# Performance work log

Hardware: AMD Instinct MI355X
Metric: run time of the kernel (lower is better)

## Reference

```python
import jax, jax.numpy as jnp
import numpy as np

EMBED = 1024
HEADS = 16
HEAD_DIM = EMBED // HEADS


def setup_inputs() -> dict:
    key = jax.random.key(0)
    ks = jax.random.split(key, 12)
    N, S, E = 4, 2048, EMBED
    scale = 1.0 / np.sqrt(E)
    inp = {
        "values": jax.random.normal(ks[0], (N, S, E), dtype=jnp.float32),
        "keys": jax.random.normal(ks[1], (N, S, E), dtype=jnp.float32),
        "query": jax.random.normal(ks[2], (N, S, E), dtype=jnp.float32),
        "mask": jnp.ones((N, 1, 1, S), dtype=jnp.int32),
        # Linear params: y = x @ W + b (W stored as [in, out])
        "Wv": jax.random.normal(ks[3], (E, E), dtype=jnp.float32) * scale,
        "bv": jnp.zeros((E,), dtype=jnp.float32),
        "Wk": jax.random.normal(ks[4], (E, E), dtype=jnp.float32) * scale,
        "bk": jnp.zeros((E,), dtype=jnp.float32),
        "Wq": jax.random.normal(ks[5], (E, E), dtype=jnp.float32) * scale,
        "bq": jnp.zeros((E,), dtype=jnp.float32),
        "Wo": jax.random.normal(ks[6], (E, E), dtype=jnp.float32) * scale,
        "bo": jnp.zeros((E,), dtype=jnp.float32),
    }
    return inp


def reference(values, keys, query, mask, Wv, bv, Wk, bk, Wq, bq, Wo, bo):
    N, Q, E = query.shape
    V = values.shape[1]
    K = keys.shape[1]
    v = (values @ Wv + bv).reshape(N, V, HEADS, HEAD_DIM)
    k = (keys @ Wk + bk).reshape(N, K, HEADS, HEAD_DIM)
    q = (query @ Wq + bq).reshape(N, Q, HEADS, HEAD_DIM)
    # energy: [N, H, Q, K]
    energy = jnp.einsum("nqhd,nkhd->nhqk", q, k)
    energy = jnp.where(mask == 0, jnp.float32(-1e20), energy)
    # NOTE: original scales by sqrt(embed_size), not sqrt(head_dim)
    attn = jax.nn.softmax(energy / jnp.sqrt(jnp.float32(E)), axis=3)
    out = jnp.einsum("nhql,nlhd->nqhd", attn, v).reshape(N, Q, E)
    return out @ Wo + bo
```

## Files before the change

### kernel.cpp

```cpp
#include <hip/hip_runtime.h>

#define H 16
#define DH 64
#define S 2048
#define E 1024
#define NB 4

typedef short short8_t __attribute__((ext_vector_type(8)));
typedef float float4_t __attribute__((ext_vector_type(4)));
typedef float float16_t __attribute__((ext_vector_type(16)));

__device__ inline unsigned short f2bf(float f) {
    union { float f; unsigned u; } v; v.f = f;
    unsigned r = v.u + 0x7fffu + ((v.u >> 16) & 1u);
    return (unsigned short)(r >> 16);
}

__device__ __forceinline__ unsigned pk_bf16(float a, float b) {
    union { float f; unsigned u; } ua, ub;
    ua.f = a; ub.f = b;
    unsigned ra = ua.u + 0x7fffu + ((ua.u >> 16) & 1u);
    unsigned rb = ub.u + 0x7fffu + ((ub.u >> 16) & 1u);
    return __builtin_amdgcn_perm(rb, ra, 0x07060302u);
}

__device__ __forceinline__ unsigned cvt_pk_bf16(float a, float b) {
    unsigned r;
    asm("v_cvt_pk_bf16_f32 %0, %1, %2" : "=v"(r) : "v"(a), "v"(b));
    return r;
}

__device__ __forceinline__ float16_t mfma32(short8_t a, short8_t b, float16_t c) {
    return __builtin_amdgcn_mfma_f32_32x32x16_bf16(a, b, c, 0, 0, 0);
}

__device__ __forceinline__ void async_copy16(const unsigned short* g, unsigned short* l) {
    __builtin_amdgcn_global_load_lds(
        (const __attribute__((address_space(1))) unsigned int*)g,
        (__attribute__((address_space(3))) unsigned int*)l, 16, 0, 0);
}

__global__ __launch_bounds__(256) void xcvt_kernel(
    const float* __restrict__ v, const float* __restrict__ k,
    const float* __restrict__ q, unsigned short* __restrict__ xv,
    unsigned short* __restrict__ xk, unsigned short* __restrict__ xq)
{
    const int z = blockIdx.y;
    const float* src = (z == 0) ? v : (z == 1) ? k : q;
    unsigned short* dst = (z == 0) ? xv : (z == 1) ? xk : xq;
    size_t i0 = ((size_t)blockIdx.x * 256 + threadIdx.x) * 8;
    float4 f0 = *reinterpret_cast<const float4*>(src + i0);
    float4 f1 = *reinterpret_cast<const float4*>(src + i0 + 4);
    uint4 o;
    o.x = pk_bf16(f0.x, f0.y); o.y = pk_bf16(f0.z, f0.w);
    o.z = pk_bf16(f1.x, f1.y); o.w = pk_bf16(f1.z, f1.w);
    *reinterpret_cast<uint4*>(dst + i0) = o;
}

__global__ __launch_bounds__(256) void wcvt_kernel(
    const float* __restrict__ Wv, const float* __restrict__ Wk,
    const float* __restrict__ Wq, const float* __restrict__ Wo,
    unsigned short* __restrict__ Wt)
{
    __shared__ float tile[64][65];
    const float* W = (blockIdx.z == 0) ? Wv : (blockIdx.z == 1) ? Wk
                   : (blockIdx.z == 2) ? Wq : Wo;
    unsigned short* out = Wt + (size_t)blockIdx.z * (E * E);
    const int k0 = blockIdx.x * 64, n0 = blockIdx.y * 64;
    const int tid = threadIdx.x;
#pragma unroll
    for (int i = 0; i < 4; ++i) {
        int c = i * 256 + tid;
        int kl = c >> 4, nl4 = (c & 15) * 4;
        float4 v = *reinterpret_cast<const float4*>(W + (size_t)(k0 + kl) * E + n0 + nl4);
        tile[kl][nl4 + 0] = v.x; tile[kl][nl4 + 1] = v.y;
        tile[kl][nl4 + 2] = v.z; tile[kl][nl4 + 3] = v.w;
    }
    __syncthreads();
#pragma unroll
    for (int i = 0; i < 4; ++i) {
        int c = i * 256 + tid;
        int nl = c >> 4, kl4 = (c & 15) * 4;
        ushort4 o;
        o.x = f2bf(tile[kl4 + 0][nl]); o.y = f2bf(tile[kl4 + 1][nl]);
        o.z = f2bf(tile[kl4 + 2][nl]); o.w = f2bf(tile[kl4 + 3][nl]);
        *reinterpret_cast<ushort4*>(out + (size_t)(n0 + nl) * E + k0 + kl4) = o;
    }
}

template<int MODE>
__global__ __launch_bounds__(256) void proj_kernel(
    const unsigned short* __restrict__ A, const unsigned short* __restrict__ WT,
    const float* __restrict__ bias, unsigned short* __restrict__ out)
{
    __shared__ __align__(16) unsigned short As[2][128][64];
    __shared__ __align__(16) unsigned short Bs[2][128][64];

    const int tid = threadIdx.x;
    const int m0 = blockIdx.y * 128;
    const int n0 = blockIdx.x * 128;
    const int wave = tid >> 6, lane = tid & 63;
    const int wm = wave >> 1, wn = wave & 1;
    const int quad = lane >> 4, l16 = lane & 15;
    const int r8 = lane >> 3;
    const int c8 = (lane & 7) ^ (r8 & 7);

    float4_t acc[4][4];
#pragma unroll
    for (int i = 0; i < 4; ++i)
#pragma unroll
        for (int j = 0; j < 4; ++j) { float4_t z = {0.f,0.f,0.f,0.f}; acc[i][j] = z; }

#pragma unroll
    for (int j = 0; j < 4; ++j) {
        int row = wave * 32 + j * 8 + r8;
        async_copy16(A  + (size_t)(m0 + row) * E + c8 * 8, &As[0][wave * 32 + j * 8][0]);
        async_copy16(WT + (size_t)(n0 + row) * E + c8 * 8, &Bs[0][wave * 32 + j * 8][0]);
    }

    for (int it = 0; it < 16; ++it) {
        const int cur = it & 1, nxt = cur ^ 1;
        __syncthreads();

        if (it < 15) {
            const int kn = (it + 1) * 64;
#pragma unroll
            for (int j = 0; j < 4; ++j) {
                int row = wave * 32 + j * 8 + r8;
                async_copy16(A  + (size_t)(m0 + row) * E + kn + c8 * 8, &As[nxt][wave * 32 + j * 8][0]);
                async_copy16(WT + (size_t)(n0 + row) * E + kn + c8 * 8, &Bs[nxt][wave * 32 + j * 8][0]);
            }
        }
#pragma unroll
        for (int kk = 0; kk < 2; ++kk) {
            short8_t a[4], b[4];
#pragma unroll
            for (int mi = 0; mi < 4; ++mi)
                a[mi] = *reinterpret_cast<const short8_t*>(
                    &As[cur][wm * 64 + mi * 16 + l16][((kk * 4 + quad) ^ (l16 & 7)) * 8]);
#pragma unroll
            for (int nj = 0; nj < 4; ++nj)
                b[nj] = *reinterpret_cast<const short8_t*>(
                    &Bs[cur][wn * 64 + nj * 16 + l16][((kk * 4 + quad) ^ (l16 & 7)) * 8]);
#pragma unroll
            for (int x = 0; x < 4; ++x)
#pragma unroll
                for (int y = 0; y < 4; ++y) {
                    if (MODE == 0)
                        acc[x][y] = __builtin_amdgcn_mfma_f32_16x16x32_bf16(b[x], a[y], acc[x][y], 0, 0, 0);
                    else
                        acc[x][y] = __builtin_amdgcn_mfma_f32_16x16x32_bf16(a[x], b[y], acc[x][y], 0, 0, 0);
                }
        }
    }

    if (MODE == 0) {
#pragma unroll
        for (int x = 0; x < 4; ++x) {
            float4 bb = *reinterpret_cast<const float4*>(&bias[n0 + wn * 64 + x * 16 + quad * 4]);
#pragma unroll
            for (int y = 0; y < 4; ++y) {
                int m = m0 + wm * 64 + y * 16 + l16;
                int nn = m >> 11, s = m & 2047;
#pragma unroll
                for (int r = 0; r < 4; ++r) {
                    int gcol = n0 + wn * 64 + x * 16 + quad * 4 + r;
                    int h = gcol >> 6, d = gcol & 63;
                    float val = acc[x][y][r] + ((const float*)&bb)[r];
                    out[(((size_t)(nn * H + h)) * DH + d) * S + s] = f2bf(val);
                }
            }
        }
    } else {
#pragma unroll
        for (int x = 0; x < 4; ++x) {
#pragma unroll
            for (int y = 0; y < 4; ++y) {
                int gcol = n0 + wn * 64 + y * 16 + l16;
                float bvv = bias[gcol];
                int h = gcol >> 6, d = gcol & 63;
#pragma unroll
                for (int r = 0; r < 4; ++r) {
                    int gm = m0 + wm * 64 + x * 16 + quad * 4 + r;
                    float val = acc[x][y][r] + bvv;
                    int nn = gm >> 11, s = gm & 2047;
                    out[(((size_t)(nn * H + h)) * S + s) * DH + d] = f2bf(val);
                }
            }
        }
    }
}

__global__ __launch_bounds__(256, 4) void flash_kernel(
    const unsigned short* __restrict__ Qb, const unsigned short* __restrict__ Kb,
    const unsigned short* __restrict__ VTb, const int* __restrict__ mask,
    unsigned short* __restrict__ AO)
{
    __shared__ __align__(16) unsigned short Ks[2][64][64];
    __shared__ __align__(16) unsigned short Vs[2][64][64];
    __shared__ __align__(16) float am[2][64];
    __shared__ __align__(16) float lbuf[4][32];

    const int tid = threadIdx.x;
    const int wave = tid >> 6, lane = tid & 63;
    const int l32 = lane & 31, hf = lane >> 5;
    const int r8 = lane >> 3;
    const int c8 = (lane & 7) ^ (r8 & 7);

    const int wlin = blockIdx.y * 16 + blockIdx.x;
    const int wid = (wlin & 7) * 128 + (wlin >> 3);
    const int qt = wid & 15;
    const int nh = wid >> 4;
    const int n = nh >> 4, h = nh & 15;
    const size_t hb = (size_t)nh * S * DH;
    const unsigned short* Qh = Qb + hb;
    const unsigned short* Kh = Kb + hb;
    const unsigned short* Vh = VTb + hb;
    const int* mp = mask + n * S;

    const float c1 = 0.03125f * 1.4426950408889634f;
    const float C2_UNMASK = -23.083120654223414f;
    const float C2_MASK   = -1.44e20f;

    short8_t qa[4];
#pragma unroll
    for (int ks = 0; ks < 4; ++ks) {
        int row = qt * 128 + wave * 32 + l32;
        qa[ks] = *reinterpret_cast<const short8_t*>(Qh + (size_t)row * DH + ks * 16 + hf * 8);
    }

    float16_t o[2];
#pragma unroll
    for (int nb = 0; nb < 2; ++nb)
#pragma unroll
        for (int i = 0; i < 16; ++i) o[nb][i] = 0.f;
    float lsum = 0.f;

#pragma unroll
    for (int j = 0; j < 2; ++j) {
        int row = wave * 16 + j * 8 + r8;
        async_copy16(Kh + (size_t)row * DH + c8 * 8, &Ks[0][wave * 16 + j * 8][0]);
        async_copy16(Vh + (size_t)row * S + c8 * 8,  &Vs[0][wave * 16 + j * 8][0]);
    }
    if (tid < 64) am[0][tid] = (mp[tid] == 0) ? C2_MASK : C2_UNMASK;

    for (int it = 0; it < 32; ++it) {
        const int cur = it & 1, nxt = cur ^ 1;
        __syncthreads();

        const int kn = (it < 31) ? (it + 1) * 64 : 0;
#pragma unroll
        for (int j = 0; j < 2; ++j) {
            int row = wave * 16 + j * 8 + r8;
            async_copy16(Kh + (size_t)(kn + row) * DH + c8 * 8, &Ks[nxt][wave * 16 + j * 8][0]);
            async_copy16(Vh + (size_t)row * S + kn + c8 * 8,    &Vs[nxt][wave * 16 + j * 8][0]);
        }
        if (tid < 64) am[nxt][tid] = (mp[kn + tid] == 0) ? C2_MASK : C2_UNMASK;

        unsigned w[2][4][2];
#pragma unroll
        for (int kvb = 0; kvb < 2; ++kvb) {
            float16_t st;
#pragma unroll
            for (int i = 0; i < 16; ++i) st[i] = 0.f;
            __builtin_amdgcn_s_setprio(1);
#pragma unroll
            for (int ks = 0; ks < 4; ++ks) {
                short8_t ak = *reinterpret_cast<const short8_t*>(
                    &Ks[cur][kvb * 32 + l32][((ks * 2 + hf) ^ (l32 & 7)) * 8]);
                st = mfma32(ak, qa[ks], st);
            }
            __builtin_amdgcn_s_setprio(0);
#pragma unroll
            for (int g = 0; g < 4; ++g) {
                float4 c2v = *reinterpret_cast<const float4*>(&am[cur][kvb * 32 + g * 8 + hf * 4]);
                float p0 = __builtin_amdgcn_exp2f(st[g * 4 + 0] * c1 + c2v.x);
                float p1 = __builtin_amdgcn_exp2f(st[g * 4 + 1] * c1 + c2v.y);
                float p2 = __builtin_amdgcn_exp2f(st[g * 4 + 2] * c1 + c2v.z);
                float p3 = __builtin_amdgcn_exp2f(st[g * 4 + 3] * c1 + c2v.w);
                lsum += (p0 + p1) + (p2 + p3);
                w[kvb][g][0] = cvt_pk_bf16(p0, p1);
                w[kvb][g][1] = cvt_pk_bf16(p2, p3);
            }
        }

        __builtin_amdgcn_s_setprio(1);
#pragma unroll
        for (int ks2 = 0; ks2 < 4; ++ks2) {
            const int kvb = ks2 >> 1, t = ks2 & 1;
            union { unsigned u[4]; short8_t s; } pu;
            pu.u[0] = w[kvb][t * 2][0];     pu.u[1] = w[kvb][t * 2][1];
            pu.u[2] = w[kvb][t * 2 + 1][0]; pu.u[3] = w[kvb][t * 2 + 1][1];
#pragma unroll
            for (int nb = 0; nb < 2; ++nb) {
                const int d = nb * 32 + l32;
                uint2 v0 = *reinterpret_cast<const uint2*>(
                    &Vs[cur][d][(((kvb * 4 + t * 2)     ) ^ (d & 7)) * 8 + hf * 4]);
                uint2 v1 = *reinterpret_cast<const uint2*>(
                    &Vs[cur][d][(((kvb * 4 + t * 2 + 1) ) ^ (d & 7)) * 8 + hf * 4]);
                union { unsigned u[4]; short8_t s; } vu;
                vu.u[0] = v0.x; vu.u[1] = v0.y; vu.u[2] = v1.x; vu.u[3] = v1.y;
                o[nb] = mfma32(pu.s, vu.s, o[nb]);
            }
        }
        __builtin_amdgcn_s_setprio(0);
    }

    lsum += __shfl_xor(lsum, 32);
    if (lane < 32) lbuf[wave][lane] = lsum;

#pragma unroll
    for (int g = 0; g < 4; ++g) {
        float4 dn = *reinterpret_cast<const float4*>(&lbuf[wave][g * 8 + hf * 4]);
#pragma unroll
        for (int r = 0; r < 4; ++r) {
            float invl = __builtin_amdgcn_rcpf(((const float*)&dn)[r]);
            int row = g * 8 + hf * 4 + r;
            int qrow = qt * 128 + wave * 32 + row;
            size_t gm = (size_t)n * S + qrow;
#pragma unroll
            for (int nb = 0; nb < 2; ++nb) {
                int col = h * DH + nb * 32 + l32;
                AO[gm * E + col] = f2bf(o[nb][g * 4 + r] * invl);
            }
        }
    }
}

__global__ __launch_bounds__(256) void ogemm_kernel(
    const unsigned short* __restrict__ A, const unsigned short* __restrict__ WT,
    const float* __restrict__ bias, float* __restrict__ out)
{
    __shared__ __align__(16) unsigned short As[2][128][64];
    __shared__ __align__(16) unsigned short Bs[2][128][64];

    const int tid = threadIdx.x;
    const int m0 = blockIdx.y * 128;
    const int n0 = blockIdx.x * 128;
    const int wave = tid >> 6, lane = tid & 63;
    const int wm = wave >> 1, wn = wave & 1;
    const int quad = lane >> 4, l16 = lane & 15;
    const int r8 = lane >> 3;
    const int c8 = (lane & 7) ^ (r8 & 7);

    float4_t acc[4][4];
#pragma unroll
    for (int i = 0; i < 4; ++i)
#pragma unroll
        for (int j = 0; j < 4; ++j) { float4_t z = {0.f,0.f,0.f,0.f}; acc[i][j] = z; }

#pragma unroll
    for (int j = 0; j < 4; ++j) {
        int row = wave * 32 + j * 8 + r8;
        async_copy16(A  + (size_t)(m0 + row) * E + c8 * 8, &As[0][wave * 32 + j * 8][0]);
        async_copy16(WT + (size_t)(n0 + row) * E + c8 * 8, &Bs[0][wave * 32 + j * 8][0]);
    }

    for (int it = 0; it < 16; ++it) {
        const int cur = it & 1, nxt = cur ^ 1;
        __syncthreads();

        if (it < 15) {
            const int kn = (it + 1) * 64;
#pragma unroll
            for (int j = 0; j < 4; ++j) {
                int row = wave * 32 + j * 8 + r8;
                async_copy16(A  + (size_t)(m0 + row) * E + kn + c8 * 8, &As[nxt][wave * 32 + j * 8][0]);
                async_copy16(WT + (size_t)(n0 + row) * E + kn + c8 * 8, &Bs[nxt][wave * 32 + j * 8][0]);
            }
        }
#pragma unroll
        for (int kk = 0; kk < 2; ++kk) {
            short8_t a[4], b[4];
#pragma unroll
            for (int mi = 0; mi < 4; ++mi)
                a[mi] = *reinterpret_cast<const short8_t*>(
                    &As[cur][wm * 64 + mi * 16 + l16][((kk * 4 + quad) ^ (l16 & 7)) * 8]);
#pragma unroll
            for (int nj = 0; nj < 4; ++nj)
                b[nj] = *reinterpret_cast<const short8_t*>(
                    &Bs[cur][wn * 64 + nj * 16 + l16][((kk * 4 + quad) ^ (l16 & 7)) * 8]);
#pragma unroll
            for (int mi = 0; mi < 4; ++mi)
#pragma unroll
                for (int nj = 0; nj < 4; ++nj)
                    acc[mi][nj] = __builtin_amdgcn_mfma_f32_16x16x32_bf16(a[mi], b[nj], acc[mi][nj], 0, 0, 0);
        }
    }
#pragma unroll
    for (int mi = 0; mi < 4; ++mi)
#pragma unroll
        for (int nj = 0; nj < 4; ++nj) {
            int gcol = n0 + wn * 64 + nj * 16 + l16;
            float bvv = bias[gcol];
#pragma unroll
            for (int r = 0; r < 4; ++r) {
                int gm = m0 + wm * 64 + mi * 16 + quad * 4 + r;
                out[(size_t)gm * E + gcol] = acc[mi][nj][r] + bvv;
            }
        }
}

extern "C" void kernel_launch(void* const* d_in, const int* in_sizes, int n_in,
                              void* d_out, int out_size, void* d_ws, size_t ws_size,
                              hipStream_t stream) {
    const float* values = (const float*)d_in[0];
    const float* keys   = (const float*)d_in[1];
    const float* query  = (const float*)d_in[2];
    const int*   mask   = (const int*)d_in[3];
    const float* Wv = (const float*)d_in[4];  const float* bv = (const float*)d_in[5];
    const float* Wk = (const float*)d_in[6];  const float* bk = (const float*)d_in[7];
    const float* Wq = (const float*)d_in[8];  const float* bq = (const float*)d_in[9];
    const float* Wo = (const float*)d_in[10]; const float* bo = (const float*)d_in[11];
    float* out = (float*)d_out;

    char* ws = (char*)d_ws;
    unsigned short* Wt = (unsigned short*)ws;
    unsigned short* xv = (unsigned short*)(ws + 8388608);
    unsigned short* xk = (unsigned short*)(ws + 25165824);
    unsigned short* xq = (unsigned short*)(ws + 41943040);
    unsigned short* vt = (unsigned short*)(ws + 58720256);
    unsigned short* kb = xv;
    unsigned short* qb = xk;
    unsigned short* ao = xq;

    xcvt_kernel<<<dim3(4096, 3), 256, 0, stream>>>(values, keys, query, xv, xk, xq);
    wcvt_kernel<<<dim3(16, 16, 4), 256, 0, stream>>>(Wv, Wk, Wq, Wo, Wt);
    proj_kernel<0><<<dim3(8, 64), 256, 0, stream>>>(xv, Wt,           bv, vt);
    proj_kernel<1><<<dim3(8, 64), 256, 0, stream>>>(xk, Wt + 1048576, bk, kb);
    proj_kernel<1><<<dim3(8, 64), 256, 0, stream>>>(xq, Wt + 2097152, bq, qb);
    flash_kernel<<<dim3(16, 64), 256, 0, stream>>>(qb, kb, vt, mask, ao);
    ogemm_kernel<<<dim3(8, 64), 256, 0, stream>>>(ao, Wt + 3145728, bo, out);
}
```

Measured before the change: 351.2 us.

## Use 8-wave GEMM blocks and permute V layout for wider LDS loads

Projection and output GEMM kernels now launch 512 threads per block, each wave computing a 32x64 sub-tile instead of 64x64, to raise parallelism and cut per-wave register pressure. The V projection store permutes sequence bits 2 and 3 so the flash kernel can fetch each V operand with a single 16-byte LDS read instead of two 8-byte reads. This trades more waves sharing the same LDS tiles and tighter register limits against better latency hiding.

```diff
diff --git a/kernel.cpp b/kernel.cpp
--- a/kernel.cpp
+++ b/kernel.cpp
@@ -89,7 +89,7 @@
 }
 
 template<int MODE>
-__global__ __launch_bounds__(256) void proj_kernel(
+__global__ __launch_bounds__(512, 4) void proj_kernel(
     const unsigned short* __restrict__ A, const unsigned short* __restrict__ WT,
     const float* __restrict__ bias, unsigned short* __restrict__ out)
 {
@@ -105,17 +105,19 @@
     const int r8 = lane >> 3;
     const int c8 = (lane & 7) ^ (r8 & 7);
 
-    float4_t acc[4][4];
-#pragma unroll
-    for (int i = 0; i < 4; ++i)
-#pragma unroll
-        for (int j = 0; j < 4; ++j) { float4_t z = {0.f,0.f,0.f,0.f}; acc[i][j] = z; }
-
-#pragma unroll
-    for (int j = 0; j < 4; ++j) {
-        int row = wave * 32 + j * 8 + r8;
-        async_copy16(A  + (size_t)(m0 + row) * E + c8 * 8, &As[0][wave * 32 + j * 8][0]);
-        async_copy16(WT + (size_t)(n0 + row) * E + c8 * 8, &Bs[0][wave * 32 + j * 8][0]);
+    constexpr int AX = (MODE == 0) ? 4 : 2;
+    constexpr int AY = (MODE == 0) ? 2 : 4;
+    float4_t acc[AX][AY];
+#pragma unroll
+    for (int i = 0; i < AX; ++i)
+#pragma unroll
+        for (int j = 0; j < AY; ++j) { float4_t z = {0.f,0.f,0.f,0.f}; acc[i][j] = z; }
+
+#pragma unroll
+    for (int j = 0; j < 2; ++j) {
+        int row = j * 64 + wave * 8 + r8;
+        async_copy16(A  + (size_t)(m0 + row) * E + c8 * 8, &As[0][j * 64 + wave * 8][0]);
+        async_copy16(WT + (size_t)(n0 + row) * E + c8 * 8, &Bs[0][j * 64 + wave * 8][0]);
     }
 
     for (int it = 0; it < 16; ++it) {
@@ -125,28 +127,28 @@
         if (it < 15) {
             const int kn = (it + 1) * 64;
 #pragma unroll
-            for (int j = 0; j < 4; ++j) {
-                int row = wave * 32 + j * 8 + r8;
-                async_copy16(A  + (size_t)(m0 + row) * E + kn + c8 * 8, &As[nxt][wave * 32 + j * 8][0]);
-                async_copy16(WT + (size_t)(n0 + row) * E + kn + c8 * 8, &Bs[nxt][wave * 32 + j * 8][0]);
+            for (int j = 0; j < 2; ++j) {
+                int row = j * 64 + wave * 8 + r8;
+                async_copy16(A  + (size_t)(m0 + row) * E + kn + c8 * 8, &As[nxt][j * 64 + wave * 8][0]);
+                async_copy16(WT + (size_t)(n0 + row) * E + kn + c8 * 8, &Bs[nxt][j * 64 + wave * 8][0]);
             }
         }
 #pragma unroll
         for (int kk = 0; kk < 2; ++kk) {
-            short8_t a[4], b[4];
-#pragma unroll
-            for (int mi = 0; mi < 4; ++mi)
+            short8_t a[2], b[4];
+#pragma unroll
+            for (int mi = 0; mi < 2; ++mi)
                 a[mi] = *reinterpret_cast<const short8_t*>(
-                    &As[cur][wm * 64 + mi * 16 + l16][((kk * 4 + quad) ^ (l16 & 7)) * 8]);
+                    &As[cur][wm * 32 + mi * 16 + l16][((kk * 4 + quad) ^ (l16 & 7)) * 8]);
 #pragma unroll
             for (int nj = 0; nj < 4; ++nj)
                 b[nj] = *reinterpret_cast<const short8_t*>(
                     &Bs[cur][wn * 64 + nj * 16 + l16][((kk * 4 + quad) ^ (l16 & 7)) * 8]);
 #pragma unroll
-            for (int x = 0; x < 4; ++x)
-#pragma unroll
-                for (int y = 0; y < 4; ++y) {
-                    if (MODE == 0)
+            for (int x = 0; x < AX; ++x)
+#pragma unroll
+                for (int y = 0; y < AY; ++y) {
+                    if constexpr (MODE == 0)
                         acc[x][y] = __builtin_amdgcn_mfma_f32_16x16x32_bf16(b[x], a[y], acc[x][y], 0, 0, 0);
                     else
                         acc[x][y] = __builtin_amdgcn_mfma_f32_16x16x32_bf16(a[x], b[y], acc[x][y], 0, 0, 0);
@@ -154,34 +156,35 @@
         }
     }
 
-    if (MODE == 0) {
-#pragma unroll
-        for (int x = 0; x < 4; ++x) {
+    if constexpr (MODE == 0) {
+#pragma unroll
+        for (int x = 0; x < AX; ++x) {
             float4 bb = *reinterpret_cast<const float4*>(&bias[n0 + wn * 64 + x * 16 + quad * 4]);
 #pragma unroll
-            for (int y = 0; y < 4; ++y) {
-                int m = m0 + wm * 64 + y * 16 + l16;
+            for (int y = 0; y < AY; ++y) {
+                int m = m0 + wm * 32 + y * 16 + l16;
                 int nn = m >> 11, s = m & 2047;
+                int sp = (s & ~12) | (((s >> 2) & 1) << 3) | (((s >> 3) & 1) << 2);
 #pragma unroll
                 for (int r = 0; r < 4; ++r) {
                     int gcol = n0 + wn * 64 + x * 16 + quad * 4 + r;
                     int h = gcol >> 6, d = gcol & 63;
                     float val = acc[x][y][r] + ((const float*)&bb)[r];
-                    out[(((size_t)(nn * H + h)) * DH + d) * S + s] = f2bf(val);
+                    out[(((size_t)(nn * H + h)) * DH + d) * S + sp] = f2bf(val);
                 }
             }
         }
     } else {
 #pragma unroll
-        for (int x = 0; x < 4; ++x) {
-#pragma unroll
-            for (int y = 0; y < 4; ++y) {
+        for (int x = 0; x < AX; ++x) {
+#pragma unroll
+            for (int y = 0; y < AY; ++y) {
                 int gcol = n0 + wn * 64 + y * 16 + l16;
                 float bvv = bias[gcol];
                 int h = gcol >> 6, d = gcol & 63;
 #pragma unroll
                 for (int r = 0; r < 4; ++r) {
-                    int gm = m0 + wm * 64 + x * 16 + quad * 4 + r;
+                    int gm = m0 + wm * 32 + x * 16 + quad * 4 + r;
                     float val = acc[x][y][r] + bvv;
                     int nn = gm >> 11, s = gm & 2047;
                     out[(((size_t)(nn * H + h)) * S + s) * DH + d] = f2bf(val);
@@ -294,13 +297,9 @@
 #pragma unroll
             for (int nb = 0; nb < 2; ++nb) {
                 const int d = nb * 32 + l32;
-                uint2 v0 = *reinterpret_cast<const uint2*>(
-                    &Vs[cur][d][(((kvb * 4 + t * 2)     ) ^ (d & 7)) * 8 + hf * 4]);
-                uint2 v1 = *reinterpret_cast<const uint2*>(
-                    &Vs[cur][d][(((kvb * 4 + t * 2 + 1) ) ^ (d & 7)) * 8 + hf * 4]);
-                union { unsigned u[4]; short8_t s; } vu;
-                vu.u[0] = v0.x; vu.u[1] = v0.y; vu.u[2] = v1.x; vu.u[3] = v1.y;
-                o[nb] = mfma32(pu.s, vu.s, o[nb]);
+                short8_t vb = *reinterpret_cast<const short8_t*>(
+                    &Vs[cur][d][((kvb * 4 + t * 2 + hf) ^ (d & 7)) * 8]);
+                o[nb] = mfma32(pu.s, vb, o[nb]);
             }
         }
         __builtin_amdgcn_s_setprio(0);
@@ -327,7 +326,7 @@
     }
 }
 
-__global__ __launch_bounds__(256) void ogemm_kernel(
+__global__ __launch_bounds__(512, 4) void ogemm_kernel(
     const unsigned short* __restrict__ A, const unsigned short* __restrict__ WT,
     const float* __restrict__ bias, float* __restrict__ out)
 {
@@ -343,17 +342,17 @@
     const int r8 = lane >> 3;
     const int c8 = (lane & 7) ^ (r8 & 7);
 
-    float4_t acc[4][4];
-#pragma unroll
-    for (int i = 0; i < 4; ++i)
+    float4_t acc[2][4];
+#pragma unroll
+    for (int i = 0; i < 2; ++i)
 #pragma unroll
         for (int j = 0; j < 4; ++j) { float4_t z = {0.f,0.f,0.f,0.f}; acc[i][j] = z; }
 
 #pragma unroll
-    for (int j = 0; j < 4; ++j) {
-        int row = wave * 32 + j * 8 + r8;
-        async_copy16(A  + (size_t)(m0 + row) * E + c8 * 8, &As[0][wave * 32 + j * 8][0]);
-        async_copy16(WT + (size_t)(n0 + row) * E + c8 * 8, &Bs[0][wave * 32 + j * 8][0]);
+    for (int j = 0; j < 2; ++j) {
+        int row = j * 64 + wave * 8 + r8;
+        async_copy16(A  + (size_t)(m0 + row) * E + c8 * 8, &As[0][j * 64 + wave * 8][0]);
+        async_copy16(WT + (size_t)(n0 + row) * E + c8 * 8, &Bs[0][j * 64 + wave * 8][0]);
     }
 
     for (int it = 0; it < 16; ++it) {
@@ -363,39 +362,39 @@
         if (it < 15) {
             const int kn = (it + 1) * 64;
 #pragma unroll
-            for (int j = 0; j < 4; ++j) {
-                int row = wave * 32 + j * 8 + r8;
-                async_copy16(A  + (size_t)(m0 + row) * E + kn + c8 * 8, &As[nxt][wave * 32 + j * 8][0]);
-                async_copy16(WT + (size_t)(n0 + row) * E + kn + c8 * 8, &Bs[nxt][wave * 32 + j * 8][0]);
+            for (int j = 0; j < 2; ++j) {
+                int row = j * 64 + wave * 8 + r8;
+                async_copy16(A  + (size_t)(m0 + row) * E + kn + c8 * 8, &As[nxt][j * 64 + wave * 8][0]);
+                async_copy16(WT + (size_t)(n0 + row) * E + kn + c8 * 8, &Bs[nxt][j * 64 + wave * 8][0]);
             }
         }
 #pragma unroll
         for (int kk = 0; kk < 2; ++kk) {
-            short8_t a[4], b[4];
-#pragma unroll
-            for (int mi = 0; mi < 4; ++mi)
+            short8_t a[2], b[4];
+#pragma unroll
+            for (int mi = 0; mi < 2; ++mi)
                 a[mi] = *reinterpret_cast<const short8_t*>(
-                    &As[cur][wm * 64 + mi * 16 + l16][((kk * 4 + quad) ^ (l16 & 7)) * 8]);
+                    &As[cur][wm * 32 + mi * 16 + l16][((kk * 4 + quad) ^ (l16 & 7)) * 8]);
 #pragma unroll
             for (int nj = 0; nj < 4; ++nj)
                 b[nj] = *reinterpret_cast<const short8_t*>(
                     &Bs[cur][wn * 64 + nj * 16 + l16][((kk * 4 + quad) ^ (l16 & 7)) * 8]);
 #pragma unroll
-            for (int mi = 0; mi < 4; ++mi)
+            for (int mi = 0; mi < 2; ++mi)
 #pragma unroll
                 for (int nj = 0; nj < 4; ++nj)
                     acc[mi][nj] = __builtin_amdgcn_mfma_f32_16x16x32_bf16(a[mi], b[nj], acc[mi][nj], 0, 0, 0);
         }
     }
 #pragma unroll
-    for (int mi = 0; mi < 4; ++mi)
+    for (int mi = 0; mi < 2; ++mi)
 #pragma unroll
         for (int nj = 0; nj < 4; ++nj) {
             int gcol = n0 + wn * 64 + nj * 16 + l16;
             float bvv = bias[gcol];
 #pragma unroll
             for (int r = 0; r < 4; ++r) {
-                int gm = m0 + wm * 64 + mi * 16 + quad * 4 + r;
+                int gm = m0 + wm * 32 + mi * 16 + quad * 4 + r;
                 out[(size_t)gm * E + gcol] = acc[mi][nj][r] + bvv;
             }
         }
@@ -426,9 +425,9 @@
 
     xcvt_kernel<<<dim3(4096, 3), 256, 0, stream>>>(values, keys, query, xv, xk, xq);
     wcvt_kernel<<<dim3(16, 16, 4), 256, 0, stream>>>(Wv, Wk, Wq, Wo, Wt);
-    proj_kernel<0><<<dim3(8, 64), 256, 0, stream>>>(xv, Wt,           bv, vt);
-    proj_kernel<1><<<dim3(8, 64), 256, 0, stream>>>(xk, Wt + 1048576, bk, kb);
-    proj_kernel<1><<<dim3(8, 64), 256, 0, stream>>>(xq, Wt + 2097152, bq, qb);
+    proj_kernel<0><<<dim3(8, 64), 512, 0, stream>>>(xv, Wt,           bv, vt);
+    proj_kernel<1><<<dim3(8, 64), 512, 0, stream>>>(xk, Wt + 1048576, bk, kb);
+    proj_kernel<1><<<dim3(8, 64), 512, 0, stream>>>(xq, Wt + 2097152, bq, qb);
     flash_kernel<<<dim3(16, 64), 256, 0, stream>>>(qb, kb, vt, mask, ao);
-    ogemm_kernel<<<dim3(8, 64), 256, 0, stream>>>(ao, Wt + 3145728, bo, out);
-}
+    ogemm_kernel<<<dim3(8, 64), 512, 0, stream>>>(ao, Wt + 3145728, bo, out);
+}
```

After: 355.7 us. No clear change (+1.3%).

## Single-buffer GEMM LDS for higher occupancy and permute V layout for wide loads

Applied to the files above, without the earlier changes.

Drops double-buffered LDS in the projection and output GEMMs in favour of a single buffer, with load, barrier, compute, barrier each iteration. It also adds a min-blocks launch bound of 3, so more blocks can fit per CU. The V projection epilogue now permutes sequence positions (swapping bits 2 and 3), which lets the attention kernel read each V fragment with one 16-byte LDS load instead of two 8-byte loads. The cost is that global-to-LDS copies no longer overlap with compute inside a block, so the change relies on other resident blocks to hide that latency.

```diff
diff --git a/kernel.cpp b/kernel.cpp
--- a/kernel.cpp
+++ b/kernel.cpp
@@ -89,12 +89,12 @@
 }
 
 template<int MODE>
-__global__ __launch_bounds__(256) void proj_kernel(
+__global__ __launch_bounds__(256, 3) void proj_kernel(
     const unsigned short* __restrict__ A, const unsigned short* __restrict__ WT,
     const float* __restrict__ bias, unsigned short* __restrict__ out)
 {
-    __shared__ __align__(16) unsigned short As[2][128][64];
-    __shared__ __align__(16) unsigned short Bs[2][128][64];
+    __shared__ __align__(16) unsigned short As[128][64];
+    __shared__ __align__(16) unsigned short Bs[128][64];
 
     const int tid = threadIdx.x;
     const int m0 = blockIdx.y * 128;
@@ -111,50 +111,40 @@
 #pragma unroll
         for (int j = 0; j < 4; ++j) { float4_t z = {0.f,0.f,0.f,0.f}; acc[i][j] = z; }
 
-#pragma unroll
-    for (int j = 0; j < 4; ++j) {
-        int row = wave * 32 + j * 8 + r8;
-        async_copy16(A  + (size_t)(m0 + row) * E + c8 * 8, &As[0][wave * 32 + j * 8][0]);
-        async_copy16(WT + (size_t)(n0 + row) * E + c8 * 8, &Bs[0][wave * 32 + j * 8][0]);
-    }
-
     for (int it = 0; it < 16; ++it) {
-        const int cur = it & 1, nxt = cur ^ 1;
+        const int kn = it * 64;
+#pragma unroll
+        for (int j = 0; j < 4; ++j) {
+            int row = wave * 32 + j * 8 + r8;
+            async_copy16(A  + (size_t)(m0 + row) * E + kn + c8 * 8, &As[wave * 32 + j * 8][0]);
+            async_copy16(WT + (size_t)(n0 + row) * E + kn + c8 * 8, &Bs[wave * 32 + j * 8][0]);
+        }
         __syncthreads();
-
-        if (it < 15) {
-            const int kn = (it + 1) * 64;
-#pragma unroll
-            for (int j = 0; j < 4; ++j) {
-                int row = wave * 32 + j * 8 + r8;
-                async_copy16(A  + (size_t)(m0 + row) * E + kn + c8 * 8, &As[nxt][wave * 32 + j * 8][0]);
-                async_copy16(WT + (size_t)(n0 + row) * E + kn + c8 * 8, &Bs[nxt][wave * 32 + j * 8][0]);
-            }
-        }
 #pragma unroll
         for (int kk = 0; kk < 2; ++kk) {
             short8_t a[4], b[4];
 #pragma unroll
             for (int mi = 0; mi < 4; ++mi)
                 a[mi] = *reinterpret_cast<const short8_t*>(
-                    &As[cur][wm * 64 + mi * 16 + l16][((kk * 4 + quad) ^ (l16 & 7)) * 8]);
+                    &As[wm * 64 + mi * 16 + l16][((kk * 4 + quad) ^ (l16 & 7)) * 8]);
 #pragma unroll
             for (int nj = 0; nj < 4; ++nj)
                 b[nj] = *reinterpret_cast<const short8_t*>(
-                    &Bs[cur][wn * 64 + nj * 16 + l16][((kk * 4 + quad) ^ (l16 & 7)) * 8]);
+                    &Bs[wn * 64 + nj * 16 + l16][((kk * 4 + quad) ^ (l16 & 7)) * 8]);
 #pragma unroll
             for (int x = 0; x < 4; ++x)
 #pragma unroll
                 for (int y = 0; y < 4; ++y) {
-                    if (MODE == 0)
+                    if constexpr (MODE == 0)
                         acc[x][y] = __builtin_amdgcn_mfma_f32_16x16x32_bf16(b[x], a[y], acc[x][y], 0, 0, 0);
                     else
                         acc[x][y] = __builtin_amdgcn_mfma_f32_16x16x32_bf16(a[x], b[y], acc[x][y], 0, 0, 0);
                 }
         }
-    }
-
-    if (MODE == 0) {
+        __syncthreads();
+    }
+
+    if constexpr (MODE == 0) {
 #pragma unroll
         for (int x = 0; x < 4; ++x) {
             float4 bb = *reinterpret_cast<const float4*>(&bias[n0 + wn * 64 + x * 16 + quad * 4]);
@@ -162,12 +152,13 @@
             for (int y = 0; y < 4; ++y) {
                 int m = m0 + wm * 64 + y * 16 + l16;
                 int nn = m >> 11, s = m & 2047;
+                int sp = (s & ~12) | (((s >> 2) & 1) << 3) | (((s >> 3) & 1) << 2);
 #pragma unroll
                 for (int r = 0; r < 4; ++r) {
                     int gcol = n0 + wn * 64 + x * 16 + quad * 4 + r;
                     int h = gcol >> 6, d = gcol & 63;
                     float val = acc[x][y][r] + ((const float*)&bb)[r];
-                    out[(((size_t)(nn * H + h)) * DH + d) * S + s] = f2bf(val);
+                    out[(((size_t)(nn * H + h)) * DH + d) * S + sp] = f2bf(val);
                 }
             }
         }
@@ -294,13 +285,9 @@
 #pragma unroll
             for (int nb = 0; nb < 2; ++nb) {
                 const int d = nb * 32 + l32;
-                uint2 v0 = *reinterpret_cast<const uint2*>(
-                    &Vs[cur][d][(((kvb * 4 + t * 2)     ) ^ (d & 7)) * 8 + hf * 4]);
-                uint2 v1 = *reinterpret_cast<const uint2*>(
-                    &Vs[cur][d][(((kvb * 4 + t * 2 + 1) ) ^ (d & 7)) * 8 + hf * 4]);
-                union { unsigned u[4]; short8_t s; } vu;
-                vu.u[0] = v0.x; vu.u[1] = v0.y; vu.u[2] = v1.x; vu.u[3] = v1.y;
-                o[nb] = mfma32(pu.s, vu.s, o[nb]);
+                short8_t vb = *reinterpret_cast<const short8_t*>(
+                    &Vs[cur][d][((kvb * 4 + t * 2 + hf) ^ (d & 7)) * 8]);
+                o[nb] = mfma32(pu.s, vb, o[nb]);
             }
         }
         __builtin_amdgcn_s_setprio(0);
@@ -327,12 +314,12 @@
     }
 }
 
-__global__ __launch_bounds__(256) void ogemm_kernel(
+__global__ __launch_bounds__(256, 3) void ogemm_kernel(
     const unsigned short* __restrict__ A, const unsigned short* __restrict__ WT,
     const float* __restrict__ bias, float* __restrict__ out)
 {
-    __shared__ __align__(16) unsigned short As[2][128][64];
-    __shared__ __align__(16) unsigned short Bs[2][128][64];
+    __shared__ __align__(16) unsigned short As[128][64];
+    __shared__ __align__(16) unsigned short Bs[128][64];
 
     const int tid = threadIdx.x;
     const int m0 = blockIdx.y * 128;
@@ -349,43 +336,33 @@
 #pragma unroll
         for (int j = 0; j < 4; ++j) { float4_t z = {0.f,0.f,0.f,0.f}; acc[i][j] = z; }
 
-#pragma unroll
-    for (int j = 0; j < 4; ++j) {
-        int row = wave * 32 + j * 8 + r8;
-        async_copy16(A  + (size_t)(m0 + row) * E + c8 * 8, &As[0][wave * 32 + j * 8][0]);
-        async_copy16(WT + (size_t)(n0 + row) * E + c8 * 8, &Bs[0][wave * 32 + j * 8][0]);
-    }
-
     for (int it = 0; it < 16; ++it) {
-        const int cur = it & 1, nxt = cur ^ 1;
+        const int kn = it * 64;
+#pragma unroll
+        for (int j = 0; j < 4; ++j) {
+            int row = wave * 32 + j * 8 + r8;
+            async_copy16(A  + (size_t)(m0 + row) * E + kn + c8 * 8, &As[wave * 32 + j * 8][0]);
+            async_copy16(WT + (size_t)(n0 + row) * E + kn + c8 * 8, &Bs[wave * 32 + j * 8][0]);
+        }
         __syncthreads();
-
-        if (it < 15) {
-            const int kn = (it + 1) * 64;
-#pragma unroll
-            for (int j = 0; j < 4; ++j) {
-                int row = wave * 32 + j * 8 + r8;
-                async_copy16(A  + (size_t)(m0 + row) * E + kn + c8 * 8, &As[nxt][wave * 32 + j * 8][0]);
-                async_copy16(WT + (size_t)(n0 + row) * E + kn + c8 * 8, &Bs[nxt][wave * 32 + j * 8][0]);
-            }
-        }
 #pragma unroll
         for (int kk = 0; kk < 2; ++kk) {
             short8_t a[4], b[4];
 #pragma unroll
             for (int mi = 0; mi < 4; ++mi)
                 a[mi] = *reinterpret_cast<const short8_t*>(
-                    &As[cur][wm * 64 + mi * 16 + l16][((kk * 4 + quad) ^ (l16 & 7)) * 8]);
+                    &As[wm * 64 + mi * 16 + l16][((kk * 4 + quad) ^ (l16 & 7)) * 8]);
 #pragma unroll
             for (int nj = 0; nj < 4; ++nj)
                 b[nj] = *reinterpret_cast<const short8_t*>(
-                    &Bs[cur][wn * 64 + nj * 16 + l16][((kk * 4 + quad) ^ (l16 & 7)) * 8]);
+                    &Bs[wn * 64 + nj * 16 + l16][((kk * 4 + quad) ^ (l16 & 7)) * 8]);
 #pragma unroll
             for (int mi = 0; mi < 4; ++mi)
 #pragma unroll
                 for (int nj = 0; nj < 4; ++nj)
                     acc[mi][nj] = __builtin_amdgcn_mfma_f32_16x16x32_bf16(a[mi], b[nj], acc[mi][nj], 0, 0, 0);
         }
+        __syncthreads();
     }
 #pragma unroll
     for (int mi = 0; mi < 4; ++mi)
```

After: 352.0 us. Within noise of the previous version (+0.2%).
